# Optimization experiments

Hardware: AMD Instinct MI355X
Metric: run time of the kernel (lower is better)

The kernel has to match this reference:

```python
import jax, jax.numpy as jnp
import numpy as np

INPUT_SIZE = 1024
HIDDEN_SIZE = 1024
BATCH = 8192


def setup_inputs() -> dict:
    key = jax.random.key(0)
    ks = jax.random.split(key, 14)
    stdv = 1.0 / HIDDEN_SIZE ** 0.5
    u = lambda k, shape: jax.random.uniform(k, shape, jnp.float32, -stdv, stdv)
    H, I = HIDDEN_SIZE, INPUT_SIZE
    return {
        "x": jax.random.normal(ks[0], (BATCH, I), jnp.float32),
        "hidden": jax.random.normal(ks[1], (BATCH, H), jnp.float32),
        "weight_xr": u(ks[2], (H, I)),
        "weight_hr": u(ks[3], (H, H)),
        "bias_r": u(ks[4], (H,)),
        "weight_xz": u(ks[5], (H, I)),
        "weight_hz": u(ks[6], (H, H)),
        "bias_z": u(ks[7], (H,)),
        "weight_xh": u(ks[8], (H, I)),
        "weight_hh": u(ks[9], (H, H)),
        "bias_h": u(ks[10], (H,)),
        "weight_c": u(ks[11], (H, I + H)),
        "bias_c": u(ks[12], (H,)),
        "weight_hat_h": u(ks[13], (H, I + H)),
        "bias_hat_h": u(jax.random.fold_in(key, 99), (H,)),
    }


def reference(x, hidden, weight_xr, weight_hr, bias_r, weight_xz, weight_hz, bias_z,
              weight_xh, weight_hh, bias_h, weight_c, bias_c, weight_hat_h, bias_hat_h):
    # combined: [B, I+H]
    combined = jnp.concatenate([x, hidden], axis=1)
    c_t = combined @ weight_c.T + bias_c                      # [B, H]
    a_t = jax.nn.softmax(c_t, axis=1)
    hat_h_t = a_t * jax.nn.relu(combined @ weight_hat_h.T + bias_hat_h)
    r_t = jax.nn.sigmoid(x @ weight_xr.T + bias_r + hidden @ weight_hr.T)
    z_t = jax.nn.sigmoid(x @ weight_xz.T + bias_z + hidden @ weight_hz.T)
    h_tilde = jnp.tanh(x @ weight_xh.T + bias_h + (r_t * hidden) @ weight_hh.T)
    h_t = (1.0 - z_t) * h_tilde + z_t * hidden + hat_h_t
    return h_t
```

## Files before the change

### kernel.cpp

```cpp
#include <hip/hip_runtime.h>

typedef unsigned short ushort_t;
typedef __attribute__((ext_vector_type(8))) short short8;
typedef __attribute__((ext_vector_type(4))) float float4v;
typedef __attribute__((ext_vector_type(4))) ushort_t ushort4v;

#define B_ROWS 8192
#define HDIM   1024
#define GLD    5120

__device__ __forceinline__ float bf2f(ushort_t u) {
    return __uint_as_float(((unsigned)u) << 16);
}
__device__ __forceinline__ ushort_t f2bf(float f) {
    unsigned u = __float_as_uint(f);
    u += 0x7FFFu + ((u >> 16) & 1u);
    return (ushort_t)(u >> 16);
}

__global__ __launch_bounds__(256) void pack_all(
    const float* __restrict__ x, const float* __restrict__ h,
    const float* __restrict__ wc, const float* __restrict__ what,
    const float* __restrict__ wxr, const float* __restrict__ whr,
    const float* __restrict__ wxz, const float* __restrict__ whz,
    const float* __restrict__ wxh, const float* __restrict__ whh,
    ushort_t* __restrict__ A, ushort_t* __restrict__ W,
    ushort_t* __restrict__ Whh)
{
    const int bid = blockIdx.x;
    float4v v;
    ushort_t* dst;
    size_t i4;
    if (bid < 16384) {
        i4 = ((size_t)bid * 256 + threadIdx.x) * 4;
        int c = (int)(i4 & 2047);
        size_t b = i4 >> 11;
        const float* src = (c < 1024) ? (x + b * 1024 + c)
                                      : (h + b * 1024 + (c - 1024));
        v = *(const float4v*)src;
        dst = A + i4;
    } else if (bid < 26624) {
        i4 = ((size_t)(bid - 16384) * 256 + threadIdx.x) * 4;
        int j = (int)(i4 >> 11);
        int k = (int)(i4 & 2047);
        int r = j >> 10, jr = j & 1023;
        if (r == 0) {
            v = *(const float4v*)(wc + (size_t)j * 2048 + k);
        } else if (r == 1) {
            v = *(const float4v*)(what + (size_t)jr * 2048 + k);
        } else if (r == 4) {
            v = (k < 1024) ? *(const float4v*)(wxh + (size_t)jr * 1024 + k)
                           : (float4v){0.f, 0.f, 0.f, 0.f};
        } else {
            const float* p0 = (r == 2) ? wxr : wxz;
            const float* p1 = (r == 2) ? whr : whz;
            const float* p = (k < 1024) ? (p0 + (size_t)jr * 1024 + k)
                                        : (p1 + (size_t)jr * 1024 + (k - 1024));
            v = *(const float4v*)p;
        }
        dst = W + i4;
    } else {
        i4 = ((size_t)(bid - 26624) * 256 + threadIdx.x) * 4;
        v = *(const float4v*)(whh + i4);
        dst = Whh + i4;
    }
    ushort4v o;
#pragma unroll
    for (int t = 0; t < 4; ++t) o[t] = f2bf(v[t]);
    *(ushort4v*)dst = o;
}

__global__ __launch_bounds__(256, 2) void gemm1(
    const ushort_t* __restrict__ A, const ushort_t* __restrict__ B,
    ushort_t* __restrict__ C)
{
    const int bn0 = blockIdx.x * 128;
    const int bm0 = blockIdx.y * 256;
    const int K = (bn0 >= 4096) ? 1024 : 2048;

    __shared__ ushort_t As[256 * 64];
    __shared__ ushort_t Bs[128 * 64];

    const int t = threadIdx.x;
    const int wave = t >> 6, lane = t & 63;
    const int q = lane >> 4, r16 = lane & 15;
    const int lrow8 = lane >> 3;
    const int kswz = ((lane & 7) ^ lrow8) * 8;
    const int xm = (r16 & 7);

    float4v acc[4][8];
#pragma unroll
    for (int i = 0; i < 4; ++i)
#pragma unroll
        for (int j = 0; j < 8; ++j)
            acc[i][j] = {0.f, 0.f, 0.f, 0.f};

    for (int k0 = 0; k0 < K; k0 += 64) {
#pragma unroll
        for (int j = 0; j < 8; ++j) {
            int l = wave * 8 + j;
            const ushort_t* gp = A + (size_t)(bm0 + l * 8 + lrow8) * 2048 + k0 + kswz;
            __builtin_amdgcn_global_load_lds(
                (const __attribute__((address_space(1))) void*)gp,
                (__attribute__((address_space(3))) void*)(As + l * 512),
                16, 0, 0);
        }
#pragma unroll
        for (int j = 0; j < 4; ++j) {
            int l = wave * 4 + j;
            const ushort_t* gp = B + (size_t)(bn0 + l * 8 + lrow8) * 2048 + k0 + kswz;
            __builtin_amdgcn_global_load_lds(
                (const __attribute__((address_space(1))) void*)gp,
                (__attribute__((address_space(3))) void*)(Bs + l * 512),
                16, 0, 0);
        }
        __syncthreads();

#pragma unroll
        for (int kh = 0; kh < 2; ++kh) {
            short8 af[4];
#pragma unroll
            for (int mi = 0; mi < 4; ++mi)
                af[mi] = *(const short8*)
                    &As[(wave * 64 + mi * 16 + r16) * 64 + (((kh * 4 + q) ^ xm) * 8)];
#pragma unroll
            for (int ni = 0; ni < 8; ++ni) {
                short8 bf = *(const short8*)
                    &Bs[(ni * 16 + r16) * 64 + (((kh * 4 + q) ^ xm) * 8)];
#pragma unroll
                for (int mi = 0; mi < 4; ++mi)
                    acc[mi][ni] = __builtin_amdgcn_mfma_f32_16x16x32_bf16(
                        af[mi], bf, acc[mi][ni], 0, 0, 0);
            }
        }
        __syncthreads();
    }

#pragma unroll
    for (int mi = 0; mi < 4; ++mi)
#pragma unroll
        for (int ni = 0; ni < 8; ++ni)
#pragma unroll
            for (int reg = 0; reg < 4; ++reg) {
                int row = bm0 + wave * 64 + mi * 16 + q * 4 + reg;
                int col = bn0 + ni * 16 + r16;
                C[(size_t)row * GLD + col] = f2bf(acc[mi][ni][reg]);
            }
}

__global__ __launch_bounds__(256) void row_pass(
    ushort_t* __restrict__ G, const float* __restrict__ bias_c,
    const float* __restrict__ bias_hat, const float* __restrict__ bias_r,
    const float* __restrict__ hidden, ushort_t* __restrict__ rh)
{
    const int wave = threadIdx.x >> 6, lane = threadIdx.x & 63;
    const size_t row = (size_t)blockIdx.x * 4 + wave;
    ushort_t* g = G + row * GLD;
    const int c0 = lane * 16;

    float cv[16];
    {
        short8 a = *(const short8*)(g + c0);
        short8 b = *(const short8*)(g + c0 + 8);
#pragma unroll
        for (int i = 0; i < 8; ++i) {
            cv[i]     = bf2f((ushort_t)a[i]) + bias_c[c0 + i];
            cv[8 + i] = bf2f((ushort_t)b[i]) + bias_c[c0 + 8 + i];
        }
    }
    float mx = cv[0];
#pragma unroll
    for (int i = 1; i < 16; ++i) mx = fmaxf(mx, cv[i]);
#pragma unroll
    for (int m = 1; m < 64; m <<= 1) mx = fmaxf(mx, __shfl_xor(mx, m));
    float sum = 0.f;
#pragma unroll
    for (int i = 0; i < 16; ++i) { cv[i] = __expf(cv[i] - mx); sum += cv[i]; }
#pragma unroll
    for (int m = 1; m < 64; m <<= 1) sum += __shfl_xor(sum, m);
    const float inv = 1.0f / sum;

    {
        short8 a = *(const short8*)(g + 1024 + c0);
        short8 b = *(const short8*)(g + 1024 + c0 + 8);
        short8 oa, ob;
#pragma unroll
        for (int i = 0; i < 8; ++i) {
            float ha = bf2f((ushort_t)a[i]) + bias_hat[c0 + i];
            float hb = bf2f((ushort_t)b[i]) + bias_hat[c0 + 8 + i];
            oa[i] = (short)f2bf(cv[i] * inv * fmaxf(ha, 0.f));
            ob[i] = (short)f2bf(cv[8 + i] * inv * fmaxf(hb, 0.f));
        }
        *(short8*)(g + c0) = oa;
        *(short8*)(g + c0 + 8) = ob;
    }

    {
        short8 a = *(const short8*)(g + 2048 + c0);
        short8 b = *(const short8*)(g + 2048 + c0 + 8);
        const float* hp = hidden + row * 1024 + c0;
        short8 oa, ob;
#pragma unroll
        for (int i = 0; i < 8; ++i) {
            float ra = 1.0f / (1.0f + __expf(-(bf2f((ushort_t)a[i]) + bias_r[c0 + i])));
            float rb = 1.0f / (1.0f + __expf(-(bf2f((ushort_t)b[i]) + bias_r[c0 + 8 + i])));
            oa[i] = (short)f2bf(ra * hp[i]);
            ob[i] = (short)f2bf(rb * hp[8 + i]);
        }
        ushort_t* rp = rh + row * 1024 + c0;
        *(short8*)rp = oa;
        *(short8*)(rp + 8) = ob;
    }
}

#define CSTRIDE 132
__global__ __launch_bounds__(256) void gemm2_final(
    const ushort_t* __restrict__ A, const ushort_t* __restrict__ B,
    const ushort_t* __restrict__ G, const float* __restrict__ bias_z,
    const float* __restrict__ bias_h, const float* __restrict__ hidden,
    float* __restrict__ out)
{
    const int bn0 = blockIdx.x * 128;
    const int bm0 = blockIdx.y * 64;

    __shared__ ushort_t smem[64 * CSTRIDE];
    ushort_t* As = smem;
    ushort_t* Bs = smem + 2048;

    const int t = threadIdx.x;
    const int wave = t >> 6, lane = t & 63;
    const int wr = wave >> 1, wcq = wave & 1;
    const int q = lane >> 4, r16 = lane & 15;
    const int lrow = lane >> 2;
    const int lcol = (lane & 3) * 8;

    float4v acc[2][4];
#pragma unroll
    for (int i = 0; i < 2; ++i)
#pragma unroll
        for (int j = 0; j < 4; ++j)
            acc[i][j] = {0.f, 0.f, 0.f, 0.f};

    for (int k0 = 0; k0 < 1024; k0 += 32) {
#pragma unroll
        for (int j = 0; j < 3; ++j) {
            int l = wave * 3 + j;
            if (l < 4) {
                const ushort_t* gp = A + (size_t)(bm0 + l * 16 + lrow) * 1024 + k0 + lcol;
                __builtin_amdgcn_global_load_lds(
                    (const __attribute__((address_space(1))) void*)gp,
                    (__attribute__((address_space(3))) void*)(As + l * 512),
                    16, 0, 0);
            } else {
                const ushort_t* gp = B + (size_t)(bn0 + (l - 4) * 16 + lrow) * 1024 + k0 + lcol;
                __builtin_amdgcn_global_load_lds(
                    (const __attribute__((address_space(1))) void*)gp,
                    (__attribute__((address_space(3))) void*)(Bs + (l - 4) * 512),
                    16, 0, 0);
            }
        }
        __syncthreads();

        short8 af[2], bf[4];
#pragma unroll
        for (int mi = 0; mi < 2; ++mi)
            af[mi] = *(const short8*)&As[(wr * 32 + mi * 16 + r16) * 32 + q * 8];
#pragma unroll
        for (int ni = 0; ni < 4; ++ni)
            bf[ni] = *(const short8*)&Bs[(wcq * 64 + ni * 16 + r16) * 32 + q * 8];
#pragma unroll
        for (int mi = 0; mi < 2; ++mi)
#pragma unroll
            for (int ni = 0; ni < 4; ++ni)
                acc[mi][ni] = __builtin_amdgcn_mfma_f32_16x16x32_bf16(
                    af[mi], bf[ni], acc[mi][ni], 0, 0, 0);
        __syncthreads();
    }

#pragma unroll
    for (int mi = 0; mi < 2; ++mi)
#pragma unroll
        for (int ni = 0; ni < 4; ++ni)
#pragma unroll
            for (int reg = 0; reg < 4; ++reg) {
                int rl = wr * 32 + mi * 16 + q * 4 + reg;
                int cl = wcq * 64 + ni * 16 + r16;
                smem[rl * CSTRIDE + cl] = f2bf(acc[mi][ni][reg]);
            }
    __syncthreads();

    const int colL = t & 127;
    const int gc = bn0 + colL;
    const float bz = bias_z[gc];
    const float bh = bias_h[gc];
    const int rbase = t >> 7;
#pragma unroll 4
    for (int pass = 0; pass < 32; ++pass) {
        const int rowL = pass * 2 + rbase;
        const size_t gr = (size_t)(bm0 + rowL);
        const ushort_t* grow = G + gr * GLD;
        float z = 1.0f / (1.0f + __expf(-(bf2f(grow[3072 + gc]) + bz)));
        float targ = bf2f(grow[4096 + gc]) + bh + bf2f(smem[rowL * CSTRIDE + colL]);
        float th = 1.0f - 2.0f / (__expf(2.0f * targ) + 1.0f);
        out[gr * 1024 + gc] =
            (1.0f - z) * th + z * hidden[gr * 1024 + gc] + bf2f(grow[gc]);
    }
}


extern "C" void kernel_launch(void* const* d_in, const int* in_sizes, int n_in,
                              void* d_out, int out_size, void* d_ws, size_t ws_size,
                              hipStream_t stream)
{
    const float* x        = (const float*)d_in[0];
    const float* hidden   = (const float*)d_in[1];
    const float* wxr      = (const float*)d_in[2];
    const float* whr      = (const float*)d_in[3];
    const float* bias_r   = (const float*)d_in[4];
    const float* wxz      = (const float*)d_in[5];
    const float* whz      = (const float*)d_in[6];
    const float* bias_z   = (const float*)d_in[7];
    const float* wxh      = (const float*)d_in[8];
    const float* whh      = (const float*)d_in[9];
    const float* bias_h   = (const float*)d_in[10];
    const float* wc       = (const float*)d_in[11];
    const float* bias_c   = (const float*)d_in[12];
    const float* what     = (const float*)d_in[13];
    const float* bias_hat = (const float*)d_in[14];
    float* out = (float*)d_out;

    char* ws = (char*)d_ws;
    ushort_t* G     = (ushort_t*)(ws);
    ushort_t* Abf   = (ushort_t*)(ws + 83886080);
    ushort_t* Wbf   = (ushort_t*)(ws + 117440512);
    ushort_t* Whhbf = (ushort_t*)(ws + 138412032);
    ushort_t* rhbf  = (ushort_t*)(ws + 140509184);

    pack_all<<<27648, 256, 0, stream>>>(x, hidden, wc, what, wxr, whr, wxz, whz,
                                        wxh, whh, Abf, Wbf, Whhbf);

    gemm1<<<dim3(40, 32), 256, 0, stream>>>(Abf, Wbf, G);

    row_pass<<<B_ROWS / 4, 256, 0, stream>>>(G, bias_c, bias_hat, bias_r, hidden, rhbf);

    gemm2_final<<<dim3(8, 128), 256, 0, stream>>>(rhbf, Whhbf, G, bias_z, bias_h,
                                                  hidden, out);
}
```

Before: 380.6 us.

## Restructure gemm1 into 256x256 tiles with a 4-stage LDS pipeline

Rewrites the first fused GEMM to use 512-thread blocks computing 256x256 output tiles, a multi-stage global_load_lds ring buffer with explicit vmcnt/lgkmcnt waits, and interleaved barriers so loads overlap with MFMA blocks. It also adds a block-ID swizzle for L2 locality, a new XOR LDS layout, and setprio around the MFMA bursts. This cuts global traffic per FLOP and hides load latency. The cost is a much larger 128 KB LDS footprint, more accumulator registers, and fragile hand-tuned wait counts.

```diff
diff --git a/kernel.cpp b/kernel.cpp
--- a/kernel.cpp
+++ b/kernel.cpp
@@ -70,80 +70,166 @@
     *(ushort4v*)dst = o;
 }
 
-__global__ __launch_bounds__(256, 2) void gemm1(
+
+#define GLOAD(gp, lp) __builtin_amdgcn_global_load_lds( \
+    (const __attribute__((address_space(1))) void*)(gp), \
+    (__attribute__((address_space(3))) void*)(lp), 16, 0, 0)
+
+#define BARRIER __builtin_amdgcn_s_barrier()
+#define WAITLGKM do { \
+    asm volatile("s_waitcnt lgkmcnt(0)" ::: "memory"); \
+    __builtin_amdgcn_sched_barrier(0); } while (0)
+#define WAITVM6 do { \
+    asm volatile("s_waitcnt vmcnt(6)" ::: "memory"); \
+    __builtin_amdgcn_sched_barrier(0); } while (0)
+#define WAITVM0 do { \
+    asm volatile("s_waitcnt vmcnt(0)" ::: "memory"); \
+    __builtin_amdgcn_sched_barrier(0); } while (0)
+
+#define LOAD_A4(OFF, MI0) \
+    _Pragma("unroll") \
+    for (int mi = 0; mi < 4; ++mi) \
+        af[mi] = *(const short8*)(Ard + (OFF) + ((MI0) + mi) * 512);
+
+#define LOAD_B4(OFF) \
+    _Pragma("unroll") \
+    for (int ni = 0; ni < 4; ++ni) \
+        bf[ni] = *(const short8*)(Brd + (OFF) + ni * 512);
+
+#define STAGE_A(KH, OFF) do { \
+    GLOAD(a_src0 + (KH) * 32, a_dst + (OFF)); \
+    GLOAD(a_src1 + (KH) * 32, a_dst + (OFF) + 4096); } while (0)
+
+#define STAGE_B(KH, OFF) do { \
+    GLOAD(b_src0 + (KH) * 32, b_dst + (OFF)); \
+    GLOAD(b_src1 + (KH) * 32, b_dst + (OFF) + 4096); } while (0)
+
+#define MFMA_BLK(R) do { \
+    __builtin_amdgcn_s_setprio(1); \
+    _Pragma("unroll") \
+    for (int mi = 0; mi < 4; ++mi) { \
+        _Pragma("unroll") \
+        for (int ni = 0; ni < 4; ++ni) \
+            acc[(R) + mi][ni] = __builtin_amdgcn_mfma_f32_16x16x32_bf16( \
+                af[mi], bf[ni], acc[(R) + mi][ni], 0, 0, 0); \
+    } \
+    __builtin_amdgcn_s_setprio(0); } while (0)
+
+__global__ __launch_bounds__(512, 2) void gemm1(
     const ushort_t* __restrict__ A, const ushort_t* __restrict__ B,
     ushort_t* __restrict__ C)
 {
-    const int bn0 = blockIdx.x * 128;
-    const int bm0 = blockIdx.y * 256;
+    const int bid = blockIdx.x;
+    const int swz = (bid & 7) * 80 + (bid >> 3);
+    const int bx = swz % 20;
+    const int by = swz / 20;
+    const int bn0 = bx * 256;
+    const int bm0 = by * 256;
     const int K = (bn0 >= 4096) ? 1024 : 2048;
-
-    __shared__ ushort_t As[256 * 64];
-    __shared__ ushort_t Bs[128 * 64];
+    const int NIT = K >> 7;
+
+    __shared__ ushort_t lds[65536];
 
     const int t = threadIdx.x;
     const int wave = t >> 6, lane = t & 63;
+    const int wm = wave >> 2, wn = wave & 3;
     const int q = lane >> 4, r16 = lane & 15;
-    const int lrow8 = lane >> 3;
-    const int kswz = ((lane & 7) ^ lrow8) * 8;
-    const int xm = (r16 & 7);
-
-    float4v acc[4][8];
-#pragma unroll
-    for (int i = 0; i < 4; ++i)
-#pragma unroll
-        for (int j = 0; j < 8; ++j)
+
+    const int s_l = (r16 & 3) ^ ((r16 >> 2) & 1);
+    const int lane_rd = r16 * 32 + ((q ^ s_l) << 3);
+    const ushort_t* Ard = lds + wm * 4096 + lane_rd;
+    const ushort_t* Brd = lds + 32768 + wn * 2048 + lane_rd;
+
+    const int srow = t >> 2;
+    const int kc = (t & 3) ^ ((t >> 2) & 3) ^ ((t >> 4) & 1);
+    const int kcOff = kc << 3;
+    const ushort_t* a_src0 = A + (size_t)(bm0 + srow) * 2048 + kcOff;
+    const ushort_t* a_src1 = a_src0 + (size_t)128 * 2048;
+    const ushort_t* b_src0 = B + (size_t)(bn0 + srow) * 2048 + kcOff;
+    const ushort_t* b_src1 = b_src0 + (size_t)128 * 2048;
+    ushort_t* a_dst = lds + wave * 512;
+    ushort_t* b_dst = lds + 32768 + wave * 512;
+
+    float4v acc[8][4];
+#pragma unroll
+    for (int i = 0; i < 8; ++i)
+#pragma unroll
+        for (int j = 0; j < 4; ++j)
             acc[i][j] = {0.f, 0.f, 0.f, 0.f};
 
-    for (int k0 = 0; k0 < K; k0 += 64) {
-#pragma unroll
-        for (int j = 0; j < 8; ++j) {
-            int l = wave * 8 + j;
-            const ushort_t* gp = A + (size_t)(bm0 + l * 8 + lrow8) * 2048 + k0 + kswz;
-            __builtin_amdgcn_global_load_lds(
-                (const __attribute__((address_space(1))) void*)gp,
-                (__attribute__((address_space(3))) void*)(As + l * 512),
-                16, 0, 0);
-        }
-#pragma unroll
-        for (int j = 0; j < 4; ++j) {
-            int l = wave * 4 + j;
-            const ushort_t* gp = B + (size_t)(bn0 + l * 8 + lrow8) * 2048 + k0 + kswz;
-            __builtin_amdgcn_global_load_lds(
-                (const __attribute__((address_space(1))) void*)gp,
-                (__attribute__((address_space(3))) void*)(Bs + l * 512),
-                16, 0, 0);
-        }
-        __syncthreads();
-
-#pragma unroll
-        for (int kh = 0; kh < 2; ++kh) {
-            short8 af[4];
-#pragma unroll
-            for (int mi = 0; mi < 4; ++mi)
-                af[mi] = *(const short8*)
-                    &As[(wave * 64 + mi * 16 + r16) * 64 + (((kh * 4 + q) ^ xm) * 8)];
-#pragma unroll
-            for (int ni = 0; ni < 8; ++ni) {
-                short8 bf = *(const short8*)
-                    &Bs[(ni * 16 + r16) * 64 + (((kh * 4 + q) ^ xm) * 8)];
-#pragma unroll
-                for (int mi = 0; mi < 4; ++mi)
-                    acc[mi][ni] = __builtin_amdgcn_mfma_f32_16x16x32_bf16(
-                        af[mi], bf, acc[mi][ni], 0, 0, 0);
-            }
-        }
-        __syncthreads();
-    }
-
-#pragma unroll
-    for (int mi = 0; mi < 4; ++mi)
-#pragma unroll
-        for (int ni = 0; ni < 8; ++ni)
+    short8 af[4], bf[4];
+
+    STAGE_A(0, 0);      STAGE_B(0, 0);
+    STAGE_A(1, 8192);   STAGE_B(1, 8192);
+    STAGE_A(2, 16384);  STAGE_B(2, 16384);
+    STAGE_B(3, 24576);
+    WAITVM6;
+    BARRIER;
+
+#pragma unroll 1
+    for (int it = 0; it < NIT - 1; ++it) {
+        const int kh0 = it << 2;
+        LOAD_A4(0, 0); LOAD_B4(0);
+        STAGE_A(kh0 + 3, 24576);
+        BARRIER; WAITLGKM; MFMA_BLK(0); BARRIER;
+        LOAD_A4(0, 4);
+        STAGE_B(kh0 + 4, 0);
+        BARRIER; WAITLGKM; MFMA_BLK(4); BARRIER;
+        LOAD_A4(8192, 0); LOAD_B4(8192);
+        STAGE_A(kh0 + 4, 0);
+        BARRIER; WAITLGKM; MFMA_BLK(0); BARRIER;
+        LOAD_A4(8192, 4);
+        STAGE_B(kh0 + 5, 8192);
+        BARRIER; WAITLGKM; MFMA_BLK(4);
+        WAITVM6;
+        BARRIER;
+        LOAD_A4(16384, 0); LOAD_B4(16384);
+        STAGE_A(kh0 + 5, 8192);
+        BARRIER; WAITLGKM; MFMA_BLK(0); BARRIER;
+        LOAD_A4(16384, 4);
+        STAGE_B(kh0 + 6, 16384);
+        BARRIER; WAITLGKM; MFMA_BLK(4); BARRIER;
+        LOAD_A4(24576, 0); LOAD_B4(24576);
+        STAGE_A(kh0 + 6, 16384);
+        BARRIER; WAITLGKM; MFMA_BLK(0); BARRIER;
+        LOAD_A4(24576, 4);
+        STAGE_B(kh0 + 7, 24576);
+        BARRIER; WAITLGKM; MFMA_BLK(4);
+        WAITVM6;
+        BARRIER;
+    }
+
+    {
+        const int kh0 = (NIT - 1) << 2;
+        LOAD_A4(0, 0); LOAD_B4(0);
+        STAGE_A(kh0 + 3, 24576);
+        BARRIER; WAITLGKM; MFMA_BLK(0); BARRIER;
+        LOAD_A4(0, 4);
+        BARRIER; WAITLGKM; MFMA_BLK(4); BARRIER;
+        LOAD_A4(8192, 0); LOAD_B4(8192);
+        BARRIER; WAITLGKM; MFMA_BLK(0); BARRIER;
+        LOAD_A4(8192, 4);
+        BARRIER; WAITLGKM; MFMA_BLK(4);
+        WAITVM0;
+        BARRIER;
+        LOAD_A4(16384, 0); LOAD_B4(16384);
+        BARRIER; WAITLGKM; MFMA_BLK(0); BARRIER;
+        LOAD_A4(16384, 4);
+        BARRIER; WAITLGKM; MFMA_BLK(4); BARRIER;
+        LOAD_A4(24576, 0); LOAD_B4(24576);
+        BARRIER; WAITLGKM; MFMA_BLK(0); BARRIER;
+        LOAD_A4(24576, 4);
+        BARRIER; WAITLGKM; MFMA_BLK(4);
+    }
+
+#pragma unroll
+    for (int mi = 0; mi < 8; ++mi)
+#pragma unroll
+        for (int ni = 0; ni < 4; ++ni)
 #pragma unroll
             for (int reg = 0; reg < 4; ++reg) {
-                int row = bm0 + wave * 64 + mi * 16 + q * 4 + reg;
-                int col = bn0 + ni * 16 + r16;
+                int row = bm0 + wm * 128 + mi * 16 + q * 4 + reg;
+                int col = bn0 + wn * 64 + ni * 16 + r16;
                 C[(size_t)row * GLD + col] = f2bf(acc[mi][ni][reg]);
             }
 }
@@ -339,7 +425,7 @@
     pack_all<<<27648, 256, 0, stream>>>(x, hidden, wc, what, wxr, whr, wxz, whz,
                                         wxh, whh, Abf, Wbf, Whhbf);
 
-    gemm1<<<dim3(40, 32), 256, 0, stream>>>(Abf, Wbf, G);
+    gemm1<<<640, 512, 0, stream>>>(Abf, Wbf, G);
 
     row_pass<<<B_ROWS / 4, 256, 0, stream>>>(G, bias_c, bias_hat, bias_r, hidden, rhbf);
 
```

Result: no change. 374.0 us (-1.7%).

## Rewrite gemm1 as 256x256 tile, 8-wave, double-buffered ping-pong pipeline

Applied to the files above, without the earlier changes.

Replaces the 256x128 single-buffered gemm1 with a 512-thread kernel computing 256x256 tiles. It double-buffers K=64 slices in 128KB of LDS using global_load_lds and interleaves the staged loads with MFMA quadrants under explicit vmcnt/lgkmcnt waits, barriers and setprio. It also remaps block IDs into a swizzled 1D grid for better L2 reuse and gives the K=1024 columns their own schedule. The aim is to hide global load latency behind MFMA work and raise arithmetic intensity. In exchange it adds fragile hand-tuned wait counts and heavy LDS use that limits occupancy.

```diff
diff --git a/kernel.cpp b/kernel.cpp
--- a/kernel.cpp
+++ b/kernel.cpp
@@ -70,82 +70,173 @@
     *(ushort4v*)dst = o;
 }
 
-__global__ __launch_bounds__(256, 2) void gemm1(
+
+#define GLOAD(gp, lp) __builtin_amdgcn_global_load_lds( \
+    (const __attribute__((address_space(1))) void*)(gp), \
+    (__attribute__((address_space(3))) void*)(lp), 16, 0, 0)
+
+#define BARRIER __builtin_amdgcn_s_barrier()
+#define WAITLGKM do { \
+    asm volatile("s_waitcnt lgkmcnt(0)" ::: "memory"); \
+    __builtin_amdgcn_sched_barrier(0); } while (0)
+#define WAITVM6 do { \
+    asm volatile("s_waitcnt vmcnt(6)" ::: "memory"); \
+    __builtin_amdgcn_sched_barrier(0); } while (0)
+#define WAITVM4 do { \
+    asm volatile("s_waitcnt vmcnt(4)" ::: "memory"); \
+    __builtin_amdgcn_sched_barrier(0); } while (0)
+#define WAITVM0 do { \
+    asm volatile("s_waitcnt vmcnt(0)" ::: "memory"); \
+    __builtin_amdgcn_sched_barrier(0); } while (0)
+
+#define STAGE_A(S, H, KT) do { \
+    GLOAD(A + aS0 + (H) * 262144 + (KT) * 64, dstA + (S) * 32768 + (H) * 8192); \
+    GLOAD(A + aS1 + (H) * 262144 + (KT) * 64, dstA + (S) * 32768 + (H) * 8192 + 512); } while (0)
+#define STAGE_B(S, H, KT) do { \
+    GLOAD(B + bS0 + (H) * 262144 + (KT) * 64, dstB + (S) * 32768 + (H) * 8192); \
+    GLOAD(B + bS1 + (H) * 262144 + (KT) * 64, dstB + (S) * 32768 + (H) * 8192 + 512); } while (0)
+
+#define LOAD_AF(S, H) do { \
+    const ushort_t* _p = lds + (S) * 32768 + (H) * 8192 + aro; \
+    _Pragma("unroll") \
+    for (int mi = 0; mi < 4; ++mi) { \
+        af0[mi] = *(const short8*)(_p + mi * 1024 + c0); \
+        af1[mi] = *(const short8*)(_p + mi * 1024 + c1); } } while (0)
+
+#define LOAD_BF(V0, V1, S, H) do { \
+    const ushort_t* _p = lds + (S) * 32768 + 16384 + (H) * 8192 + bro; \
+    _Pragma("unroll") \
+    for (int ni = 0; ni < 2; ++ni) { \
+        V0[ni] = *(const short8*)(_p + ni * 1024 + c0); \
+        V1[ni] = *(const short8*)(_p + ni * 1024 + c1); } } while (0)
+
+#define MFMA_Q(HA, HB, V0, V1) do { \
+    __builtin_amdgcn_s_setprio(1); \
+    _Pragma("unroll") \
+    for (int mi = 0; mi < 4; ++mi) { \
+        _Pragma("unroll") \
+        for (int ni = 0; ni < 2; ++ni) { \
+            acc[HA][HB][mi][ni] = __builtin_amdgcn_mfma_f32_16x16x32_bf16( \
+                af0[mi], V0[ni], acc[HA][HB][mi][ni], 0, 0, 0); \
+            acc[HA][HB][mi][ni] = __builtin_amdgcn_mfma_f32_16x16x32_bf16( \
+                af1[mi], V1[ni], acc[HA][HB][mi][ni], 0, 0, 0); } } \
+    __builtin_amdgcn_s_setprio(0); } while (0)
+
+__global__ __launch_bounds__(512, 2) void gemm1(
     const ushort_t* __restrict__ A, const ushort_t* __restrict__ B,
     ushort_t* __restrict__ C)
 {
-    const int bn0 = blockIdx.x * 128;
-    const int bm0 = blockIdx.y * 256;
-    const int K = (bn0 >= 4096) ? 1024 : 2048;
-
-    __shared__ ushort_t As[256 * 64];
-    __shared__ ushort_t Bs[128 * 64];
+    const int bid = blockIdx.x;
+    int bx, by;
+    if (bid < 512) { int hI = (bid & 7) * 64 + (bid >> 3); by = hI >> 4; bx = hI & 15; }
+    else           { int b = bid - 512; int lI = (b & 7) * 16 + (b >> 3); by = lI >> 2; bx = 16 + (lI & 3); }
+    const int bn0 = bx * 256;
+    const int bm0 = by * 256;
+    const int K = (bx >= 16) ? 1024 : 2048;
+    const int NIT = K >> 7;
+
+    __shared__ ushort_t lds[65536];
 
     const int t = threadIdx.x;
-    const int wave = t >> 6, lane = t & 63;
+    const int w = t >> 6, lane = t & 63;
+    const int wm2 = w >> 2, wn2 = w & 3;
     const int q = lane >> 4, r16 = lane & 15;
-    const int lrow8 = lane >> 3;
-    const int kswz = ((lane & 7) ^ lrow8) * 8;
-    const int xm = (r16 & 7);
-
-    float4v acc[4][8];
-#pragma unroll
-    for (int i = 0; i < 4; ++i)
-#pragma unroll
-        for (int j = 0; j < 8; ++j)
-            acc[i][j] = {0.f, 0.f, 0.f, 0.f};
-
-    for (int k0 = 0; k0 < K; k0 += 64) {
-#pragma unroll
-        for (int j = 0; j < 8; ++j) {
-            int l = wave * 8 + j;
-            const ushort_t* gp = A + (size_t)(bm0 + l * 8 + lrow8) * 2048 + k0 + kswz;
-            __builtin_amdgcn_global_load_lds(
-                (const __attribute__((address_space(1))) void*)gp,
-                (__attribute__((address_space(3))) void*)(As + l * 512),
-                16, 0, 0);
-        }
-#pragma unroll
-        for (int j = 0; j < 4; ++j) {
-            int l = wave * 4 + j;
-            const ushort_t* gp = B + (size_t)(bn0 + l * 8 + lrow8) * 2048 + k0 + kswz;
-            __builtin_amdgcn_global_load_lds(
-                (const __attribute__((address_space(1))) void*)gp,
-                (__attribute__((address_space(3))) void*)(Bs + l * 512),
-                16, 0, 0);
-        }
-        __syncthreads();
-
-#pragma unroll
-        for (int kh = 0; kh < 2; ++kh) {
-            short8 af[4];
+
+    const int c0 = ((q ^ (r16 & 7)) << 3);
+    const int c1 = (((4 + q) ^ (r16 & 7)) << 3);
+    const int aro = (wm2 * 64 + r16) * 64;
+    const int bro = (wn2 * 32 + r16) * 64;
+
+    const int srow0 = w * 16 + ((lane >> 3) & 7);
+    const int kcO = ((lane & 7) ^ (lane >> 3)) << 3;
+    const size_t aS0 = (size_t)(bm0 + srow0) * 2048 + kcO;
+    const size_t aS1 = aS0 + 8 * 2048;
+    const size_t bS0 = (size_t)(bn0 + srow0) * 2048 + kcO;
+    const size_t bS1 = bS0 + 8 * 2048;
+    ushort_t* dstA = lds + w * 1024;
+    ushort_t* dstB = lds + 16384 + w * 1024;
+
+    float4v acc[2][2][4][2];
+#pragma unroll
+    for (int i = 0; i < 2; ++i)
+#pragma unroll
+        for (int j = 0; j < 2; ++j)
+#pragma unroll
+            for (int m = 0; m < 4; ++m)
+#pragma unroll
+                for (int n = 0; n < 2; ++n)
+                    acc[i][j][m][n] = {0.f, 0.f, 0.f, 0.f};
+
+    short8 af0[4], af1[4];
+    short8 b00[2], b01[2];
+    short8 b10[2], b11[2];
+
+    STAGE_A(0, 0, 0);
+    STAGE_B(0, 0, 0);
+    STAGE_A(0, 1, 0);
+    STAGE_B(0, 1, 0);
+    STAGE_A(1, 0, 1);
+    STAGE_B(1, 1, 1);
+    WAITVM4;
+    BARRIER;
+
+#pragma unroll 1
+    for (int it = 0; it < NIT - 1; ++it) {
+        const int kO  = 2 * it + 1;
+        const int kE2 = 2 * it + 2;
+        const int kO2 = 2 * it + 3;
+        LOAD_AF(0, 0); LOAD_BF(b00, b01, 0, 0); STAGE_B(1, 0, kO);
+        BARRIER; WAITLGKM; MFMA_Q(0, 0, b00, b01); WAITVM6; BARRIER;
+        LOAD_BF(b10, b11, 0, 1); STAGE_A(1, 1, kO);
+        BARRIER; WAITLGKM; MFMA_Q(0, 1, b10, b11); WAITVM6; BARRIER;
+        LOAD_AF(0, 1); STAGE_A(0, 0, kE2);
+        BARRIER; WAITLGKM; MFMA_Q(1, 1, b10, b11); WAITVM6; BARRIER;
+        STAGE_B(0, 1, kE2);
+        BARRIER; MFMA_Q(1, 0, b00, b01); WAITVM6; BARRIER;
+        LOAD_AF(1, 0); LOAD_BF(b00, b01, 1, 0); STAGE_B(0, 0, kE2);
+        BARRIER; WAITLGKM; MFMA_Q(0, 0, b00, b01); WAITVM6; BARRIER;
+        LOAD_BF(b10, b11, 1, 1); STAGE_A(0, 1, kE2);
+        BARRIER; WAITLGKM; MFMA_Q(0, 1, b10, b11); WAITVM6; BARRIER;
+        LOAD_AF(1, 1); STAGE_A(1, 0, kO2);
+        BARRIER; WAITLGKM; MFMA_Q(1, 1, b10, b11); WAITVM6; BARRIER;
+        STAGE_B(1, 1, kO2);
+        BARRIER; MFMA_Q(1, 0, b00, b01); WAITVM6; BARRIER;
+    }
+
+    {
+        const int kO = 2 * (NIT - 1) + 1;
+        LOAD_AF(0, 0); LOAD_BF(b00, b01, 0, 0); STAGE_B(1, 0, kO);
+        BARRIER; WAITLGKM; MFMA_Q(0, 0, b00, b01); WAITVM6; BARRIER;
+        LOAD_BF(b10, b11, 0, 1); STAGE_A(1, 1, kO);
+        BARRIER; WAITLGKM; MFMA_Q(0, 1, b10, b11); WAITVM6; BARRIER;
+        LOAD_AF(0, 1);
+        WAITLGKM; MFMA_Q(1, 1, b10, b11);
+        MFMA_Q(1, 0, b00, b01);
+        WAITVM0;
+        BARRIER;
+        LOAD_AF(1, 0); LOAD_BF(b00, b01, 1, 0);
+        WAITLGKM; MFMA_Q(0, 0, b00, b01);
+        LOAD_BF(b10, b11, 1, 1);
+        WAITLGKM; MFMA_Q(0, 1, b10, b11);
+        LOAD_AF(1, 1);
+        WAITLGKM; MFMA_Q(1, 1, b10, b11);
+        MFMA_Q(1, 0, b00, b01);
+    }
+
+#pragma unroll
+    for (int ha = 0; ha < 2; ++ha)
+#pragma unroll
+        for (int hb = 0; hb < 2; ++hb)
 #pragma unroll
             for (int mi = 0; mi < 4; ++mi)
-                af[mi] = *(const short8*)
-                    &As[(wave * 64 + mi * 16 + r16) * 64 + (((kh * 4 + q) ^ xm) * 8)];
-#pragma unroll
-            for (int ni = 0; ni < 8; ++ni) {
-                short8 bf = *(const short8*)
-                    &Bs[(ni * 16 + r16) * 64 + (((kh * 4 + q) ^ xm) * 8)];
-#pragma unroll
-                for (int mi = 0; mi < 4; ++mi)
-                    acc[mi][ni] = __builtin_amdgcn_mfma_f32_16x16x32_bf16(
-                        af[mi], bf, acc[mi][ni], 0, 0, 0);
-            }
-        }
-        __syncthreads();
-    }
-
-#pragma unroll
-    for (int mi = 0; mi < 4; ++mi)
-#pragma unroll
-        for (int ni = 0; ni < 8; ++ni)
-#pragma unroll
-            for (int reg = 0; reg < 4; ++reg) {
-                int row = bm0 + wave * 64 + mi * 16 + q * 4 + reg;
-                int col = bn0 + ni * 16 + r16;
-                C[(size_t)row * GLD + col] = f2bf(acc[mi][ni][reg]);
-            }
+#pragma unroll
+                for (int ni = 0; ni < 2; ++ni)
+#pragma unroll
+                    for (int reg = 0; reg < 4; ++reg) {
+                        int row = bm0 + ha * 128 + wm2 * 64 + mi * 16 + q * 4 + reg;
+                        int col = bn0 + hb * 128 + wn2 * 32 + ni * 16 + r16;
+                        C[(size_t)row * GLD + col] = f2bf(acc[ha][hb][mi][ni][reg]);
+                    }
 }
 
 __global__ __launch_bounds__(256) void row_pass(
@@ -339,7 +430,7 @@
     pack_all<<<27648, 256, 0, stream>>>(x, hidden, wc, what, wxr, whr, wxz, whz,
                                         wxh, whh, Abf, Wbf, Whhbf);
 
-    gemm1<<<dim3(40, 32), 256, 0, stream>>>(Abf, Wbf, G);
+    gemm1<<<640, 512, 0, stream>>>(Abf, Wbf, G);
 
     row_pass<<<B_ROWS / 4, 256, 0, stream>>>(G, bias_c, bias_hat, bias_r, hidden, rhbf);
 
```

Measured after the change: 358.3 us. 1.06x faster.
